# Kernel tuning notes

Hardware: AMD Instinct MI355X
Metric: run time of the kernel (lower is better)

The kernel has to match this reference:

```python
import jax, jax.numpy as jnp
import numpy as np

BLOCK_SIZE = 256
EMB = 384
HEAD = 64
B = 256
T = 256

def setup_inputs() -> dict:
    key = jax.random.key(0)
    k1, k2, k3, k4 = jax.random.split(key, 4)
    x = jax.random.normal(k1, (B, T, EMB), dtype=jnp.float32)
    # torch Linear(no bias) default init ~ U(-1/sqrt(in), 1/sqrt(in)); use scaled normal
    s = 1.0 / np.sqrt(EMB)
    Wq = jax.random.normal(k2, (EMB, HEAD), dtype=jnp.float32) * s
    Wk = jax.random.normal(k3, (EMB, HEAD), dtype=jnp.float32) * s
    Wv = jax.random.normal(k4, (EMB, HEAD), dtype=jnp.float32) * s
    return {"x": x, "Wq": Wq, "Wk": Wk, "Wv": Wv}

def reference(x, Wq, Wk, Wv):
    Bb, Tt, C = x.shape
    q = jnp.einsum('btc,ch->bth', x, Wq)
    k = jnp.einsum('btc,ch->bth', x, Wk)
    v = jnp.einsum('btc,ch->bth', x, Wv)
    # NOTE: source scales by C**-0.5 where C = embedding dim (384), not head_size
    scores = jnp.einsum('bth,bsh->bts', q, k) * (C ** -0.5)  # [B,T,T]
    causal = jnp.tril(jnp.ones((Tt, Tt), dtype=bool))
    scores = jnp.where(causal, scores, -jnp.inf)
    weights = jax.nn.softmax(scores, axis=-1)
    # dropout is identity in eval mode (reference baseline)
    out = jnp.einsum('bts,bsh->bth', weights, v)
    return out
```

## Files before the change

kernel.cpp:

```cpp
#include <hip/hip_runtime.h>
#include <hip/hip_bf16.h>
#include <cstdint>
#include <cstddef>

#define B_DIM 256
#define T_DIM 256
#define EMB   384
#define HEAD  64

typedef __attribute__((ext_vector_type(8))) short bf16x8;
typedef __attribute__((ext_vector_type(4))) float f32x4;
typedef __attribute__((ext_vector_type(4))) unsigned int u32x4;

__device__ __forceinline__ unsigned short f2bf(float f) {
    union { float f; unsigned int u; } v; v.f = f;
    unsigned int r = v.u + 0x7fffu + ((v.u >> 16) & 1u);
    return (unsigned short)(r >> 16);
}

__device__ __forceinline__ unsigned int pkbf(float a, float b) {
#if __has_builtin(__builtin_amdgcn_cvt_pk_bf16_f32)
    typedef __attribute__((ext_vector_type(2))) __bf16 bf16x2_t;
    bf16x2_t r = __builtin_amdgcn_cvt_pk_bf16_f32(a, b);
    return *(unsigned int*)&r;
#else
    return (unsigned)f2bf(a) | ((unsigned)f2bf(b) << 16);
#endif
}

__global__ void wprep_kernel(const float* __restrict__ Wq, const float* __restrict__ Wk,
                             const float* __restrict__ Wv, unsigned short* __restrict__ Wb) {
    int g = blockIdx.x * blockDim.x + threadIdx.x;
    if (g >= 9216) return;
    int kkstep = g / 1536, rem = g - kkstep * 1536;
    int r = rem >> 3, cs = rem & 7, c = cs ^ (r & 7);
    const float* W = (r < 64) ? Wq : (r < 128) ? Wk : Wv;
    int h = r & 63;
    unsigned short tmp[8];
#pragma unroll
    for (int e = 0; e < 8; ++e) {
        int k = kkstep * 64 + c * 8 + e;
        tmp[e] = f2bf(W[k * HEAD + h]);
    }
    *(u32x4*)(Wb + (size_t)g * 8) = *(u32x4*)tmp;
}

__global__ __launch_bounds__(512, 1) void fused_kernel(const float* __restrict__ x,
                                                       const unsigned short* __restrict__ Wb,
                                                       float* __restrict__ out) {
    __shared__ union SM {
        struct { unsigned short Xs[2][256][72]; unsigned short Ws[2][12288]; } p1;
        struct { unsigned short qs[256][72]; unsigned short ks[256][72];
                 unsigned short vT[64][264]; unsigned short Ps[8][16][72]; } p2;
    } sm;

    const int tid = threadIdx.x;
    const int w = tid >> 6, lane = tid & 63, qd = lane >> 4, l15 = lane & 15;
    const int mh = w >> 1, nh = w & 1;
    const int b = blockIdx.x;
    const float* xb = x + (size_t)b * T_DIM * EMB;
    const int r = tid >> 1, h = tid & 1;

#pragma unroll
    for (int s = 0; s < 3; ++s) {
        int idx = s * 512 + w * 64;
        const unsigned short* gp = Wb + (size_t)(idx + lane) * 8;
        unsigned short* lp = &sm.p1.Ws[0][idx * 8];
        __builtin_amdgcn_global_load_lds(
            (const __attribute__((address_space(1))) unsigned int*)gp,
            (__attribute__((address_space(3))) unsigned int*)lp, 16, 0, 0);
    }

    const float* xp = xb + (size_t)r * EMB + h * 64;
    float4 xf[3][8];
    unsigned int st0[32], st1[32], st2[32];

#define LOADC(BUF, C) do { \
    _Pragma("unroll") \
    for (int ii = 0; ii < 8; ++ii) \
        xf[BUF][ii] = *(const float4*)(xp + ((C) >> 1) * 128 + ((C) & 1) * 32 + ii * 4); \
} while (0)

#define CONVC(BUF, ST, C) do { \
    _Pragma("unroll") \
    for (int ii = 0; ii < 8; ++ii) { \
        ST[16 * ((C) & 1) + 2 * ii]     = pkbf(xf[BUF][ii].x, xf[BUF][ii].y); \
        ST[16 * ((C) & 1) + 2 * ii + 1] = pkbf(xf[BUF][ii].z, xf[BUF][ii].w); \
    } \
} while (0)

#define SCATTER(ST, S) do { \
    if (h == ((S) & 1)) { \
        _Pragma("unroll") \
        for (int q = 0; q < 8; ++q) \
            *(u32x4*)&sm.p1.Xs[(S) & 1][r][8 * q] = \
                (u32x4){ST[4 * q], ST[4 * q + 1], ST[4 * q + 2], ST[4 * q + 3]}; \
    } \
} while (0)

    LOADC(0, 0); LOADC(1, 1); LOADC(2, 2);
    CONVC(0, st0, 0); LOADC(0, 3);
    CONVC(1, st0, 1); LOADC(1, 4);
    SCATTER(st0, 0);
    SCATTER(st0, 1);
    CONVC(2, st1, 2); LOADC(2, 5);
    CONVC(0, st1, 3);
    CONVC(1, st2, 4);
    CONVC(2, st2, 5);

    f32x4 acc[4][6];
#pragma unroll
    for (int mt = 0; mt < 4; ++mt)
#pragma unroll
        for (int nt = 0; nt < 6; ++nt) acc[mt][nt] = (f32x4){0.f, 0.f, 0.f, 0.f};

#pragma unroll
    for (int kk = 0; kk < 6; ++kk) {
        __syncthreads();
        if (kk < 5) {
#pragma unroll
            for (int s = 0; s < 3; ++s) {
                int idx = s * 512 + w * 64;
                const unsigned short* gp = Wb + (size_t)((kk + 1) * 1536 + idx + lane) * 8;
                unsigned short* lp = &sm.p1.Ws[(kk + 1) & 1][idx * 8];
                __builtin_amdgcn_global_load_lds(
                    (const __attribute__((address_space(1))) unsigned int*)gp,
                    (__attribute__((address_space(3))) unsigned int*)lp, 16, 0, 0);
            }
        }
#pragma unroll
        for (int kb = 0; kb < 2; ++kb) {
            bf16x8 a[4], bb[6];
#pragma unroll
            for (int mt = 0; mt < 4; ++mt)
                a[mt] = *(const bf16x8*)&sm.p1.Xs[kk & 1][64 * mh + 16 * mt + l15][32 * kb + 8 * qd];
#pragma unroll
            for (int nt = 0; nt < 6; ++nt) {
                int n = 96 * nh + 16 * nt + l15;
                bb[nt] = *(const bf16x8*)&sm.p1.Ws[kk & 1][n * 64 + (((4 * kb + qd) ^ (n & 7)) << 3)];
            }
#pragma unroll
            for (int mt = 0; mt < 4; ++mt)
#pragma unroll
                for (int nt = 0; nt < 6; ++nt)
                    acc[mt][nt] = __builtin_amdgcn_mfma_f32_16x16x32_bf16(a[mt], bb[nt], acc[mt][nt], 0, 0, 0);
        }
        if (kk == 1) SCATTER(st1, 2);
        if (kk == 2) SCATTER(st1, 3);
        if (kk == 3) SCATTER(st2, 4);
        if (kk == 4) SCATTER(st2, 5);
    }
    __syncthreads();

#pragma unroll
    for (int nt = 0; nt < 6; ++nt) {
        int n = 96 * nh + 16 * nt + l15;
        int arr = n >> 6, hh = n & 63;
        if (arr == 2) {
#pragma unroll
            for (int mt = 0; mt < 4; ++mt) {
                int tok0 = 64 * mh + 16 * mt + 4 * qd;
                *(uint2*)&sm.p2.vT[hh][tok0] = make_uint2(
                    pkbf(acc[mt][nt][0], acc[mt][nt][1]),
                    pkbf(acc[mt][nt][2], acc[mt][nt][3]));
            }
        } else {
#pragma unroll
            for (int mt = 0; mt < 4; ++mt)
#pragma unroll
                for (int reg = 0; reg < 4; ++reg) {
                    int tok = 64 * mh + 16 * mt + 4 * qd + reg;
                    unsigned short val = f2bf(acc[mt][nt][reg]);
                    if (arr == 0) sm.p2.qs[tok][hh] = val;
                    else          sm.p2.ks[tok][hh] = val;
                }
        }
    }
    __syncthreads();

    const int tiles[2] = { w, 15 - w };
    bf16x8 aq[2][2];
#pragma unroll
    for (int ti = 0; ti < 2; ++ti)
#pragma unroll
        for (int kbi = 0; kbi < 2; ++kbi)
            aq[ti][kbi] = *(const bf16x8*)&sm.p2.qs[16 * tiles[ti] + l15][32 * kbi + 8 * qd];

    f32x4 O[2][4];
    float l[2][4];
#pragma unroll
    for (int ti = 0; ti < 2; ++ti) {
#pragma unroll
        for (int dn = 0; dn < 4; ++dn) O[ti][dn] = (f32x4){0.f, 0.f, 0.f, 0.f};
#pragma unroll
        for (int reg = 0; reg < 4; ++reg) l[ti][reg] = 0.f;
    }

    const float cExp = 1.4426950408889634f / 19.595917942265423f;

#pragma unroll
    for (int ti = 0; ti < 2; ++ti) {
        const int t = tiles[ti];
        for (int jc = 0; jc <= (t >> 2); ++jc) {
            const int ntmax = min(3, t - 4 * jc);
            f32x4 S[4];
#pragma unroll
            for (int nt = 0; nt < 4; ++nt) {
                if (nt <= ntmax) {
                    bf16x8 b0 = *(const bf16x8*)&sm.p2.ks[64 * jc + 16 * nt + l15][8 * qd];
                    bf16x8 b1 = *(const bf16x8*)&sm.p2.ks[64 * jc + 16 * nt + l15][32 + 8 * qd];
                    f32x4 s = __builtin_amdgcn_mfma_f32_16x16x32_bf16(aq[ti][0], b0, (f32x4){0.f,0.f,0.f,0.f}, 0, 0, 0);
                    s = __builtin_amdgcn_mfma_f32_16x16x32_bf16(aq[ti][1], b1, s, 0, 0, 0);
                    S[nt] = s;
                }
            }
#pragma unroll
            for (int nt = 0; nt < 4; ++nt) {
#pragma unroll
                for (int reg = 0; reg < 4; ++reg) {
                    float p = 0.0f;
                    if (nt <= ntmax) {
                        p = exp2f(S[nt][reg] * cExp);
                        if (4 * jc + nt == t && (l15 > 4 * qd + reg)) p = 0.0f;
                    }
                    l[ti][reg] += p;
                    sm.p2.Ps[w][4 * qd + reg][16 * nt + l15] = f2bf(p);
                }
            }
            bf16x8 ap0 = *(const bf16x8*)&sm.p2.Ps[w][l15][8 * qd];
            bf16x8 ap1 = *(const bf16x8*)&sm.p2.Ps[w][l15][32 + 8 * qd];
#pragma unroll
            for (int dn = 0; dn < 4; ++dn) {
                bf16x8 bv0 = *(const bf16x8*)&sm.p2.vT[16 * dn + l15][64 * jc + 8 * qd];
                bf16x8 bv1 = *(const bf16x8*)&sm.p2.vT[16 * dn + l15][64 * jc + 32 + 8 * qd];
                O[ti][dn] = __builtin_amdgcn_mfma_f32_16x16x32_bf16(ap0, bv0, O[ti][dn], 0, 0, 0);
                O[ti][dn] = __builtin_amdgcn_mfma_f32_16x16x32_bf16(ap1, bv1, O[ti][dn], 0, 0, 0);
            }
        }
    }

#pragma unroll
    for (int ti = 0; ti < 2; ++ti) {
#pragma unroll
        for (int reg = 0; reg < 4; ++reg) {
            float s = l[ti][reg];
            s += __shfl_xor(s, 1);
            s += __shfl_xor(s, 2);
            s += __shfl_xor(s, 4);
            s += __shfl_xor(s, 8);
            float inv = 1.0f / s;
            int row = 16 * tiles[ti] + 4 * qd + reg;
            float* dst = out + ((size_t)b * T_DIM + row) * HEAD;
#pragma unroll
            for (int dn = 0; dn < 4; ++dn)
                dst[16 * dn + l15] = O[ti][dn][reg] * inv;
        }
    }
}

extern "C" void kernel_launch(void* const* d_in, const int* in_sizes, int n_in,
                              void* d_out, int out_size, void* d_ws, size_t ws_size,
                              hipStream_t stream) {
    const float* x  = (const float*)d_in[0];
    const float* Wq = (const float*)d_in[1];
    const float* Wk = (const float*)d_in[2];
    const float* Wv = (const float*)d_in[3];
    float* out = (float*)d_out;

    unsigned short* Wb = (unsigned short*)d_ws;

    wprep_kernel<<<36, 256, 0, stream>>>(Wq, Wk, Wv, Wb);
    fused_kernel<<<B_DIM, 512, 0, stream>>>(x, Wb, out);
}
```

Before: 187.1 us.

## Restructure QKV projection into two 128-row passes with full-K x staging

The QKV projection now runs in two passes of 128 tokens each. For each pass the whole 384-wide x slab is loaded, converted to bf16 and written into a swizzled LDS buffer up front, instead of streaming 64-wide K chunks with register-staged scatter. The warp grid changes from 4x2 to 2x4, so each warp does 4x3 MFMA tiles per pass. W tiles are re-streamed for each pass, which removes the interleaved load/convert/scatter pipeline and its register pressure. The cost is reloading W twice and losing overlap between x loads and MFMAs, since x for a pass is fully loaded before compute starts.

```diff
diff --git a/kernel.cpp b/kernel.cpp
--- a/kernel.cpp
+++ b/kernel.cpp
@@ -49,133 +49,121 @@
                                                        const unsigned short* __restrict__ Wb,
                                                        float* __restrict__ out) {
     __shared__ union SM {
-        struct { unsigned short Xs[2][256][72]; unsigned short Ws[2][12288]; } p1;
+        struct { unsigned short Xst[6][128][64]; unsigned short Ws[2][12288]; } p1;
         struct { unsigned short qs[256][72]; unsigned short ks[256][72];
                  unsigned short vT[64][264]; unsigned short Ps[8][16][72]; } p2;
     } sm;
 
     const int tid = threadIdx.x;
     const int w = tid >> 6, lane = tid & 63, qd = lane >> 4, l15 = lane & 15;
-    const int mh = w >> 1, nh = w & 1;
+    const int wm = w >> 2, wn = w & 3;
     const int b = blockIdx.x;
     const float* xb = x + (size_t)b * T_DIM * EMB;
-    const int r = tid >> 1, h = tid & 1;
-
-#pragma unroll
-    for (int s = 0; s < 3; ++s) {
-        int idx = s * 512 + w * 64;
-        const unsigned short* gp = Wb + (size_t)(idx + lane) * 8;
-        unsigned short* lp = &sm.p1.Ws[0][idx * 8];
-        __builtin_amdgcn_global_load_lds(
-            (const __attribute__((address_space(1))) unsigned int*)gp,
-            (__attribute__((address_space(3))) unsigned int*)lp, 16, 0, 0);
-    }
-
-    const float* xp = xb + (size_t)r * EMB + h * 64;
-    float4 xf[3][8];
-    unsigned int st0[32], st1[32], st2[32];
-
-#define LOADC(BUF, C) do { \
+    const int trow = tid >> 4, fc = tid & 15;
+
+#define WGLDS(KSTEP, BUF) do { \
     _Pragma("unroll") \
-    for (int ii = 0; ii < 8; ++ii) \
-        xf[BUF][ii] = *(const float4*)(xp + ((C) >> 1) * 128 + ((C) & 1) * 32 + ii * 4); \
-} while (0)
-
-#define CONVC(BUF, ST, C) do { \
-    _Pragma("unroll") \
-    for (int ii = 0; ii < 8; ++ii) { \
-        ST[16 * ((C) & 1) + 2 * ii]     = pkbf(xf[BUF][ii].x, xf[BUF][ii].y); \
-        ST[16 * ((C) & 1) + 2 * ii + 1] = pkbf(xf[BUF][ii].z, xf[BUF][ii].w); \
+    for (int s = 0; s < 3; ++s) { \
+        int idx = s * 512 + w * 64; \
+        const unsigned short* gp = Wb + (size_t)((KSTEP) * 1536 + idx + lane) * 8; \
+        unsigned short* lp = &sm.p1.Ws[BUF][idx * 8]; \
+        __builtin_amdgcn_global_load_lds( \
+            (const __attribute__((address_space(1))) unsigned int*)gp, \
+            (__attribute__((address_space(3))) unsigned int*)lp, 16, 0, 0); \
     } \
 } while (0)
 
-#define SCATTER(ST, S) do { \
-    if (h == ((S) & 1)) { \
-        _Pragma("unroll") \
-        for (int q = 0; q < 8; ++q) \
-            *(u32x4*)&sm.p1.Xs[(S) & 1][r][8 * q] = \
-                (u32x4){ST[4 * q], ST[4 * q + 1], ST[4 * q + 2], ST[4 * q + 3]}; \
+#define XLOAD(P, RG) do { \
+    _Pragma("unroll") \
+    for (int kk = 0; kk < 6; ++kk) \
+        xq[(RG) & 1][kk] = *(const float4*)(xb + (size_t)((P) * 128 + (RG) * 32 + trow) * EMB + kk * 64 + 4 * fc); \
+} while (0)
+
+#define XCW(RG) do { \
+    int row_ = (RG) * 32 + trow; \
+    _Pragma("unroll") \
+    for (int kk = 0; kk < 6; ++kk) { \
+        float4 v_ = xq[(RG) & 1][kk]; \
+        *(uint2*)((char*)&sm.p1.Xst[kk][row_][0] + ((((fc >> 1) ^ (row_ & 7)) << 4) | ((fc & 1) << 3))) = \
+            make_uint2(pkbf(v_.x, v_.y), pkbf(v_.z, v_.w)); \
     } \
 } while (0)
 
-    LOADC(0, 0); LOADC(1, 1); LOADC(2, 2);
-    CONVC(0, st0, 0); LOADC(0, 3);
-    CONVC(1, st0, 1); LOADC(1, 4);
-    SCATTER(st0, 0);
-    SCATTER(st0, 1);
-    CONVC(2, st1, 2); LOADC(2, 5);
-    CONVC(0, st1, 3);
-    CONVC(1, st2, 4);
-    CONVC(2, st2, 5);
-
-    f32x4 acc[4][6];
-#pragma unroll
-    for (int mt = 0; mt < 4; ++mt)
-#pragma unroll
-        for (int nt = 0; nt < 6; ++nt) acc[mt][nt] = (f32x4){0.f, 0.f, 0.f, 0.f};
-
-#pragma unroll
-    for (int kk = 0; kk < 6; ++kk) {
+    f32x4 acc[2][4][3];
+#pragma unroll
+    for (int P = 0; P < 2; ++P)
+#pragma unroll
+        for (int mt = 0; mt < 4; ++mt)
+#pragma unroll
+            for (int nt = 0; nt < 3; ++nt) acc[P][mt][nt] = (f32x4){0.f, 0.f, 0.f, 0.f};
+
+    float4 xq[2][6];
+
+#pragma unroll
+    for (int P = 0; P < 2; ++P) {
+        WGLDS(0, 0);
+        XLOAD(P, 0); XLOAD(P, 1);
+        XCW(0);
+        XLOAD(P, 2);
+        XCW(1);
+        XLOAD(P, 3);
+        XCW(2);
+        XCW(3);
+
+#pragma unroll
+        for (int kk = 0; kk < 6; ++kk) {
+            __syncthreads();
+            if (kk < 5) WGLDS(kk + 1, (kk + 1) & 1);
+#pragma unroll
+            for (int kb = 0; kb < 2; ++kb) {
+                bf16x8 a[4], bb[3];
+#pragma unroll
+                for (int mt = 0; mt < 4; ++mt) {
+                    int rl = 64 * wm + 16 * mt + l15;
+                    a[mt] = *(const bf16x8*)((const char*)&sm.p1.Xst[kk][rl][0] +
+                                             ((((kb << 2) + qd) ^ (rl & 7)) << 4));
+                }
+#pragma unroll
+                for (int nt = 0; nt < 3; ++nt) {
+                    int n = 48 * wn + 16 * nt + l15;
+                    bb[nt] = *(const bf16x8*)&sm.p1.Ws[kk & 1][n * 64 + (((4 * kb + qd) ^ (n & 7)) << 3)];
+                }
+#pragma unroll
+                for (int mt = 0; mt < 4; ++mt)
+#pragma unroll
+                    for (int nt = 0; nt < 3; ++nt)
+                        acc[P][mt][nt] = __builtin_amdgcn_mfma_f32_16x16x32_bf16(a[mt], bb[nt], acc[P][mt][nt], 0, 0, 0);
+            }
+        }
         __syncthreads();
-        if (kk < 5) {
-#pragma unroll
-            for (int s = 0; s < 3; ++s) {
-                int idx = s * 512 + w * 64;
-                const unsigned short* gp = Wb + (size_t)((kk + 1) * 1536 + idx + lane) * 8;
-                unsigned short* lp = &sm.p1.Ws[(kk + 1) & 1][idx * 8];
-                __builtin_amdgcn_global_load_lds(
-                    (const __attribute__((address_space(1))) unsigned int*)gp,
-                    (__attribute__((address_space(3))) unsigned int*)lp, 16, 0, 0);
-            }
-        }
-#pragma unroll
-        for (int kb = 0; kb < 2; ++kb) {
-            bf16x8 a[4], bb[6];
-#pragma unroll
-            for (int mt = 0; mt < 4; ++mt)
-                a[mt] = *(const bf16x8*)&sm.p1.Xs[kk & 1][64 * mh + 16 * mt + l15][32 * kb + 8 * qd];
-#pragma unroll
-            for (int nt = 0; nt < 6; ++nt) {
-                int n = 96 * nh + 16 * nt + l15;
-                bb[nt] = *(const bf16x8*)&sm.p1.Ws[kk & 1][n * 64 + (((4 * kb + qd) ^ (n & 7)) << 3)];
-            }
-#pragma unroll
-            for (int mt = 0; mt < 4; ++mt)
-#pragma unroll
-                for (int nt = 0; nt < 6; ++nt)
-                    acc[mt][nt] = __builtin_amdgcn_mfma_f32_16x16x32_bf16(a[mt], bb[nt], acc[mt][nt], 0, 0, 0);
-        }
-        if (kk == 1) SCATTER(st1, 2);
-        if (kk == 2) SCATTER(st1, 3);
-        if (kk == 3) SCATTER(st2, 4);
-        if (kk == 4) SCATTER(st2, 5);
-    }
-    __syncthreads();
-
-#pragma unroll
-    for (int nt = 0; nt < 6; ++nt) {
-        int n = 96 * nh + 16 * nt + l15;
-        int arr = n >> 6, hh = n & 63;
-        if (arr == 2) {
-#pragma unroll
-            for (int mt = 0; mt < 4; ++mt) {
-                int tok0 = 64 * mh + 16 * mt + 4 * qd;
-                *(uint2*)&sm.p2.vT[hh][tok0] = make_uint2(
-                    pkbf(acc[mt][nt][0], acc[mt][nt][1]),
-                    pkbf(acc[mt][nt][2], acc[mt][nt][3]));
-            }
-        } else {
-#pragma unroll
-            for (int mt = 0; mt < 4; ++mt)
-#pragma unroll
-                for (int reg = 0; reg < 4; ++reg) {
-                    int tok = 64 * mh + 16 * mt + 4 * qd + reg;
-                    unsigned short val = f2bf(acc[mt][nt][reg]);
-                    if (arr == 0) sm.p2.qs[tok][hh] = val;
-                    else          sm.p2.ks[tok][hh] = val;
-                }
-        }
-    }
+    }
+
+#pragma unroll
+    for (int P = 0; P < 2; ++P)
+#pragma unroll
+        for (int nt = 0; nt < 3; ++nt) {
+            int n = 48 * wn + 16 * nt + l15;
+            int arr = n >> 6, hh = n & 63;
+            if (arr == 2) {
+#pragma unroll
+                for (int mt = 0; mt < 4; ++mt) {
+                    int tok0 = 128 * P + 64 * wm + 16 * mt + 4 * qd;
+                    *(uint2*)&sm.p2.vT[hh][tok0] = make_uint2(
+                        pkbf(acc[P][mt][nt][0], acc[P][mt][nt][1]),
+                        pkbf(acc[P][mt][nt][2], acc[P][mt][nt][3]));
+                }
+            } else {
+#pragma unroll
+                for (int mt = 0; mt < 4; ++mt)
+#pragma unroll
+                    for (int reg = 0; reg < 4; ++reg) {
+                        int tok = 128 * P + 64 * wm + 16 * mt + 4 * qd + reg;
+                        unsigned short val = f2bf(acc[P][mt][nt][reg]);
+                        if (arr == 0) sm.p2.qs[tok][hh] = val;
+                        else          sm.p2.ks[tok][hh] = val;
+                    }
+            }
+        }
     __syncthreads();
 
     const int tiles[2] = { w, 15 - w };
```

New measurement: 173.8 us. -7.1%, faster.
